# Kernel tuning notes

Hardware: AMD Instinct MI355X
Metric: run time of the kernel (lower is better)

The kernel has to match this reference:

```python
import jax, jax.numpy as jnp
import numpy as np


def _xcorr3x3_valid(x, k):
    # x: [B,H,W], k: [B,3,3] per-sample kernel; cross-correlation (matches F.conv2d), VALID padding
    B, H, W = x.shape
    out = jnp.zeros((B, H - 2, W - 2), dtype=x.dtype)
    for u in range(3):
        for v in range(3):
            out = out + x[:, u:u + H - 2, v:v + W - 2] * k[:, u, v, None, None]
    return out


def setup_inputs() -> dict:
    key = jax.random.key(0)
    ks = jax.random.split(key, 4)
    B, H, W = 256, 256, 256
    pred = jax.random.normal(ks[0], (B, H, W), dtype=jnp.float32)
    rhs = jax.random.normal(ks[1], (B, H - 2, W - 2), dtype=jnp.float32)
    Laplace_kernel = jax.random.normal(ks[2], (B, 3, 3), dtype=jnp.float32)
    Df_dr_kernel = jax.random.normal(ks[3], (B, 3, 3), dtype=jnp.float32)
    # physically sensible meshgrids: R in [1,2] (avoids div-by-zero), Z in [-1,1]
    r = jnp.linspace(1.0, 2.0, W, dtype=jnp.float32)
    z = jnp.linspace(-1.0, 1.0, H, dtype=jnp.float32)
    RR = jnp.broadcast_to(r[None, None, :], (B, H, W)).astype(jnp.float32)
    ZZ = jnp.broadcast_to(z[None, :, None], (B, H, W)).astype(jnp.float32)
    Gauss_kernel = (jnp.array([[1., 2., 1.], [2., 4., 2.], [1., 2., 1.]], dtype=jnp.float32) / 16.0)
    return {"pred": pred, "rhs": rhs, "Laplace_kernel": Laplace_kernel,
            "Df_dr_kernel": Df_dr_kernel, "RR": RR, "ZZ": ZZ, "Gauss_kernel": Gauss_kernel}


def reference(pred, rhs, Laplace_kernel, Df_dr_kernel, RR, ZZ, Gauss_kernel):
    # Lpsi, Dpsi_dr: per-sample 3x3 VALID stencils -> [B, H-2, W-2]
    Lpsi = _xcorr3x3_valid(pred, Laplace_kernel)
    Dpsi_dr = -_xcorr3x3_valid(pred, Df_dr_kernel)
    Dpsi_dr = Dpsi_dr / RR[:, 1:-1, 1:-1]
    lhs = Lpsi - Dpsi_dr
    hr = (RR[:, 1, 2] - RR[:, 1, 1])[:, None, None]
    hz = (ZZ[:, 2, 1] - ZZ[:, 1, 1])[:, None, None]
    alfa = -2.0 * (hr ** 2 + hz ** 2)
    GS_ope = lhs * alfa / (hr ** 2 * hz ** 2)
    # Gaussian smoothing, shared kernel, SAME padding (cross-correlation; kernel is symmetric)
    sm = jax.lax.conv_general_dilated(
        GS_ope[:, None, :, :], Gauss_kernel[None, None, :, :],
        window_strides=(1, 1), padding='SAME')
    GS_ope_smooth = -sm
    rhs_computed = -GS_ope_smooth[:, 0, :, :]
    return jnp.mean((rhs_computed - rhs) ** 2)
```

## Files before the change

kernel.cpp:

```cpp
#include <hip/hip_runtime.h>


__global__ __launch_bounds__(256, 4)
void pde_loss_kernel(const float* __restrict__ pred,
                     const float* __restrict__ rhs,
                     const float* __restrict__ KL,
                     const float* __restrict__ KD,
                     const float* __restrict__ RR,
                     const float* __restrict__ ZZ,
                     float* __restrict__ out,
                     float inv_n)
{
    constexpr int H = 256, W = 256, OH = 254, OW = 254;
    const int tid = threadIdx.x;
    const int l   = tid & 63;
    const int wv  = tid >> 6;
    const int b   = blockIdx.x >> 3;
    const int strip = (blockIdx.x & 7) * 4 + wv;
    const int o0 = strip * 8;
    const int o1 = (o0 + 8 < OH) ? (o0 + 8) : OH;

    const size_t ib = (size_t)b * H * W;
    const float* predb = pred + ib;
    const float* rhsb  = rhs + (size_t)b * OH * OW;

    const float hr  = RR[ib + W + 2] - RR[ib + W + 1];
    const float hz  = ZZ[ib + 2 * W + 1] - ZZ[ib + W + 1];
    const float hr2 = hr * hr, hz2 = hz * hz;
    const float s   = -2.0f * (hr2 + hz2) / (hr2 * hz2);

    const int c0 = 4 * l;
    float4 c4[9];
    {
        float4 invr;
        invr.x = 1.0f / RR[ib + W + (c0 + 1)];
        invr.y = 1.0f / RR[ib + W + (c0 + 2)];
        invr.z = 1.0f / RR[ib + W + (c0 + 3)];
        invr.w = 1.0f / RR[ib + W + ((c0 + 4 < W) ? (c0 + 4) : (W - 1))];
        const float* kl = KL + b * 9;
        const float* kd = KD + b * 9;
#pragma unroll
        for (int t = 0; t < 9; ++t) {
            const float a = kl[t] * s, d = kd[t] * s;
            c4[t].x = fmaf(d, invr.x, a);
            c4[t].y = fmaf(d, invr.y, a);
            c4[t].z = fmaf(d, invr.z, a);
            c4[t].w = fmaf(d, invr.w, a);
        }
    }

    const int g0 = o0 - 1;
    float4 pa = make_float4(0.f, 0.f, 0.f, 0.f), pb, pc;
    if (g0 >= 0) pa = *(const float4*)(predb + (size_t)g0 * W + c0);
    pb = *(const float4*)(predb + (size_t)(g0 + 1) * W + c0);
    pc = *(const float4*)(predb + (size_t)(g0 + 2) * W + c0);
    float nxa = __shfl(pa.x, l + 1, 64), nya = __shfl(pa.y, l + 1, 64);
    float nxb = __shfl(pb.x, l + 1, 64), nyb = __shfl(pb.y, l + 1, 64);

    float4 ghA = make_float4(0.f, 0.f, 0.f, 0.f);
    float4 ghB = make_float4(0.f, 0.f, 0.f, 0.f);
    float2 rc0 = make_float2(0.f, 0.f), rc1 = make_float2(0.f, 0.f);
    float acc = 0.0f;

    for (int g = g0; g <= o1; ++g) {
        float4 pn = make_float4(0.f, 0.f, 0.f, 0.f);
        const int rowp = g + 3;
        if (rowp < H && rowp <= o1 + 2)
            pn = *(const float4*)(predb + (size_t)rowp * W + c0);

        float2 rn0 = make_float2(0.f, 0.f), rn1 = make_float2(0.f, 0.f);
        if (g >= o0 && g < o1) {
            const float* rrow = rhsb + (size_t)g * OW + c0;
            rn0 = *(const float2*)rrow;
            if (c0 + 2 < OW) rn1 = *(const float2*)(rrow + 2);
        }

        const float nxc = __shfl(pc.x, l + 1, 64);
        const float nyc = __shfl(pc.y, l + 1, 64);

        float4 gs = make_float4(0.f, 0.f, 0.f, 0.f);
        if ((unsigned)g < (unsigned)OH) {
#define ROWC(p, nx, ny, t0)                                              \
            gs.x = fmaf(p.x, c4[t0].x, fmaf(p.y, c4[t0+1].x, fmaf(p.z, c4[t0+2].x, gs.x))); \
            gs.y = fmaf(p.y, c4[t0].y, fmaf(p.z, c4[t0+1].y, fmaf(p.w, c4[t0+2].y, gs.y))); \
            gs.z = fmaf(p.z, c4[t0].z, fmaf(p.w, c4[t0+1].z, fmaf(nx,  c4[t0+2].z, gs.z))); \
            gs.w = fmaf(p.w, c4[t0].w, fmaf(nx,  c4[t0+1].w, fmaf(ny,  c4[t0+2].w, gs.w)));
            ROWC(pa, nxa, nya, 0)
            ROWC(pb, nxb, nyb, 3)
            ROWC(pc, nxc, nyc, 6)
#undef ROWC
            if (l == 63) { gs.z = 0.f; gs.w = 0.f; }
        }

        float up = __shfl(gs.w, l - 1, 64);
        const float dn = __shfl(gs.x, l + 1, 64);
        if (l == 0) up = 0.f;
        float4 gh;
        gh.x = fmaf(2.f, gs.x, up   + gs.y);
        gh.y = fmaf(2.f, gs.y, gs.x + gs.z);
        gh.z = fmaf(2.f, gs.z, gs.y + gs.w);
        gh.w = fmaf(2.f, gs.w, gs.z + dn);

        const int i = g - 1;
        if (i >= o0 && i < o1) {
            const float smx = (ghA.x + 2.f * ghB.x + gh.x) * 0.0625f;
            const float smy = (ghA.y + 2.f * ghB.y + gh.y) * 0.0625f;
            const float smz = (ghA.z + 2.f * ghB.z + gh.z) * 0.0625f;
            const float smw = (ghA.w + 2.f * ghB.w + gh.w) * 0.0625f;
            const float dx = smx - rc0.x;
            const float dy = smy - rc0.y;
            float dz = smz - rc1.x;
            float dw = smw - rc1.y;
            if (c0 + 2 >= OW) { dz = 0.f; dw = 0.f; }
            acc = fmaf(dx, dx, acc);
            acc = fmaf(dy, dy, acc);
            acc = fmaf(dz, dz, acc);
            acc = fmaf(dw, dw, acc);
        }

        pa = pb; pb = pc; pc = pn;
        nxa = nxb; nya = nyb; nxb = nxc; nyb = nyc;
        ghA = ghB; ghB = gh;
        rc0 = rn0; rc1 = rn1;
    }

#pragma unroll
    for (int off = 32; off > 0; off >>= 1)
        acc += __shfl_down(acc, off, 64);
    __shared__ float wsum[4];
    if (l == 0) wsum[wv] = acc;
    __syncthreads();
    if (tid == 0) {
        const float t = (wsum[0] + wsum[1]) + (wsum[2] + wsum[3]);
        atomicAdd(out, t * inv_n);
    }
}

extern "C" void kernel_launch(void* const* d_in, const int* in_sizes, int n_in,
                              void* d_out, int out_size, void* d_ws, size_t ws_size,
                              hipStream_t stream) {
    const float* pred = (const float*)d_in[0];
    const float* rhs  = (const float*)d_in[1];
    const float* KL   = (const float*)d_in[2];
    const float* KD   = (const float*)d_in[3];
    const float* RR   = (const float*)d_in[4];
    const float* ZZ   = (const float*)d_in[5];
    float* out = (float*)d_out;

    const int B = in_sizes[2] / 9;
    const float inv_n = 1.0f / ((float)B * 254.0f * 254.0f);

    hipMemsetAsync(out, 0, sizeof(float), stream);
    pde_loss_kernel<<<dim3(B * 8), dim3(256), 0, stream>>>(pred, rhs, KL, KD, RR, ZZ, out, inv_n);
}
```

Before: 228.2 us.

## Stage pred and rhs row tiles in LDS with 16-row blocks

```diff
diff --git a/kernel.cpp b/kernel.cpp
--- a/kernel.cpp
+++ b/kernel.cpp
@@ -15,14 +15,36 @@
     const int tid = threadIdx.x;
     const int l   = tid & 63;
     const int wv  = tid >> 6;
-    const int b   = blockIdx.x >> 3;
-    const int strip = (blockIdx.x & 7) * 4 + wv;
-    const int o0 = strip * 8;
-    const int o1 = (o0 + 8 < OH) ? (o0 + 8) : OH;
+    const int b   = blockIdx.x >> 4;
+    const int o0T = (blockIdx.x & 15) * 16;
+
+    __shared__ float predT[20][256];
+    __shared__ float rhsT[16][256];
+    __shared__ float wsum[4];
 
     const size_t ib = (size_t)b * H * W;
     const float* predb = pred + ib;
     const float* rhsb  = rhs + (size_t)b * OH * OW;
+
+#pragma unroll
+    for (int k = 0; k < 5; ++k) {
+        const int idx = tid + k * 256;
+        const int tr = idx >> 6, cq = idx & 63;
+        const int gr = o0T - 1 + tr;
+        if (gr >= 0 && gr < H)
+            *(float4*)&predT[tr][cq * 4] = *(const float4*)(predb + (size_t)gr * W + cq * 4);
+    }
+#pragma unroll
+    for (int k = 0; k < 4; ++k) {
+        const int idx = tid + k * 256;
+        const int tr = idx >> 6, cq = idx & 63;
+        const int ro = o0T + tr;
+        if (ro < OH) {
+            const float* src = rhsb + (size_t)ro * OW + cq * 4;
+            if (cq < 63) *(float4*)&rhsT[tr][cq * 4] = *(const float4*)src;
+            else         *(float2*)&rhsT[tr][252]    = *(const float2*)src;
+        }
+    }
 
     const float hr  = RR[ib + W + 2] - RR[ib + W + 1];
     const float hz  = ZZ[ib + 2 * W + 1] - ZZ[ib + W + 1];
@@ -49,31 +71,28 @@
         }
     }
 
+    __syncthreads();
+
+    const int o0 = o0T + 4 * wv;
+    const int o1 = (o0 + 4 < OH) ? (o0 + 4) : OH;
+
     const int g0 = o0 - 1;
     float4 pa = make_float4(0.f, 0.f, 0.f, 0.f), pb, pc;
-    if (g0 >= 0) pa = *(const float4*)(predb + (size_t)g0 * W + c0);
-    pb = *(const float4*)(predb + (size_t)(g0 + 1) * W + c0);
-    pc = *(const float4*)(predb + (size_t)(g0 + 2) * W + c0);
+    if (g0 >= 0) pa = *(const float4*)&predT[g0 - o0T + 1][c0];
+    pb = *(const float4*)&predT[g0 - o0T + 2][c0];
+    pc = *(const float4*)&predT[g0 - o0T + 3][c0];
     float nxa = __shfl(pa.x, l + 1, 64), nya = __shfl(pa.y, l + 1, 64);
     float nxb = __shfl(pb.x, l + 1, 64), nyb = __shfl(pb.y, l + 1, 64);
 
     float4 ghA = make_float4(0.f, 0.f, 0.f, 0.f);
     float4 ghB = make_float4(0.f, 0.f, 0.f, 0.f);
-    float2 rc0 = make_float2(0.f, 0.f), rc1 = make_float2(0.f, 0.f);
     float acc = 0.0f;
 
     for (int g = g0; g <= o1; ++g) {
         float4 pn = make_float4(0.f, 0.f, 0.f, 0.f);
         const int rowp = g + 3;
         if (rowp < H && rowp <= o1 + 2)
-            pn = *(const float4*)(predb + (size_t)rowp * W + c0);
-
-        float2 rn0 = make_float2(0.f, 0.f), rn1 = make_float2(0.f, 0.f);
-        if (g >= o0 && g < o1) {
-            const float* rrow = rhsb + (size_t)g * OW + c0;
-            rn0 = *(const float2*)rrow;
-            if (c0 + 2 < OW) rn1 = *(const float2*)(rrow + 2);
-        }
+            pn = *(const float4*)&predT[rowp - o0T + 1][c0];
 
         const float nxc = __shfl(pc.x, l + 1, 64);
         const float nyc = __shfl(pc.y, l + 1, 64);
@@ -103,14 +122,15 @@
 
         const int i = g - 1;
         if (i >= o0 && i < o1) {
+            const float4 r = *(const float4*)&rhsT[i - o0T][c0];
             const float smx = (ghA.x + 2.f * ghB.x + gh.x) * 0.0625f;
             const float smy = (ghA.y + 2.f * ghB.y + gh.y) * 0.0625f;
             const float smz = (ghA.z + 2.f * ghB.z + gh.z) * 0.0625f;
             const float smw = (ghA.w + 2.f * ghB.w + gh.w) * 0.0625f;
-            const float dx = smx - rc0.x;
-            const float dy = smy - rc0.y;
-            float dz = smz - rc1.x;
-            float dw = smw - rc1.y;
+            const float dx = smx - r.x;
+            const float dy = smy - r.y;
+            float dz = smz - r.z;
+            float dw = smw - r.w;
             if (c0 + 2 >= OW) { dz = 0.f; dw = 0.f; }
             acc = fmaf(dx, dx, acc);
             acc = fmaf(dy, dy, acc);
@@ -121,13 +141,11 @@
         pa = pb; pb = pc; pc = pn;
         nxa = nxb; nya = nyb; nxb = nxc; nyb = nyc;
         ghA = ghB; ghB = gh;
-        rc0 = rn0; rc1 = rn1;
     }
 
 #pragma unroll
     for (int off = 32; off > 0; off >>= 1)
         acc += __shfl_down(acc, off, 64);
-    __shared__ float wsum[4];
     if (l == 0) wsum[wv] = acc;
     __syncthreads();
     if (tid == 0) {
@@ -151,5 +169,5 @@
     const float inv_n = 1.0f / ((float)B * 254.0f * 254.0f);
 
     hipMemsetAsync(out, 0, sizeof(float), stream);
-    pde_loss_kernel<<<dim3(B * 8), dim3(256), 0, stream>>>(pred, rhs, KL, KD, RR, ZZ, out, inv_n);
+    pde_loss_kernel<<<dim3(B * 16), dim3(256), 0, stream>>>(pred, rhs, KL, KD, RR, ZZ, out, inv_n);
 }
```

New measurement: 245.7 us. +7.6%, slower.
